# Kernel tuning notes

Measured on AMD Instinct MI355X. Metric: run time of the kernel, lower is better.

The kernel has to match this reference:

```python
import jax, jax.numpy as jnp
import numpy as np

EMBED = 768; HEADS = 12; MLP = 3072
WL_IN = 4        # activation bits (signed)
WL_W = 4         # weight bits (bit-sliced into 1-bit RRAM cells)
ADC = 5          # ADC precision for each analog partial sum
SUBARRAY = 128   # crossbar subArray rows
ONOFF = 10.0     # conductance on/off ratio
VARI = 0.02      # conductance variability
EPS = 1e-5


def _adc_quant(y, bits):
    # Linear ADC quantization over the full observed range.
    ymax = jnp.max(jnp.abs(y))
    step = ymax / (2 ** bits - 1)
    step = jnp.where(step > 0, step, jnp.ones_like(step))
    return jnp.round(y / step) * step


def _qlinear(x, W, b, key):
    # RRAM crossbar simulated linear layer. x: [T, Fin], W: [Fout, Fin].
    upper, lower = 1.0, 1.0 / ONOFF
    T, Fin = x.shape
    Fout = W.shape[0]
    Wlev = 2 ** WL_W - 1
    Xlev = 2 ** (WL_IN - 1) - 1
    # --- weight -> unsigned integer levels -> binary cell conductances ---
    wmax = jnp.max(jnp.abs(W))
    Wdec = jnp.round((W / wmax + 1.0) * 0.5 * Wlev).astype(jnp.int32)   # [Fout,Fin] in [0,Wlev]
    kb = jnp.arange(WL_W)
    wbits = ((Wdec[:, :, None] >> kb) & 1).astype(x.dtype)              # [Fout,Fin,K]
    noise = VARI * jax.random.normal(key, wbits.shape, dtype=x.dtype)   # conductance variability
    cond = (wbits * (upper - lower) + lower) * (1.0 + noise)
    dummy = 0.5 * (upper + lower)                                       # dummy column conductance
    # --- activation -> signed integer -> magnitude bit slices ---
    xmax = jnp.max(jnp.abs(x))
    Xq = jnp.round(x / xmax * Xlev).astype(jnp.int32)
    sgn = jnp.sign(Xq).astype(x.dtype)
    zb = jnp.arange(WL_IN - 1)
    xbits = ((jnp.abs(Xq)[:, :, None] >> zb) & 1).astype(x.dtype) * sgn[:, :, None]  # [T,Fin,Z]
    # --- subArray partitioning along input dim ---
    pad = (-Fin) % SUBARRAY
    if pad:
        xbits = jnp.pad(xbits, ((0, 0), (0, pad), (0, 0)))
        cond = jnp.pad(cond, ((0, 0), (0, pad), (0, 0)))
    nc = (Fin + pad) // SUBARRAY
    xb = xbits.reshape(T, nc, SUBARRAY, WL_IN - 1)
    cb = cond.reshape(Fout, nc, SUBARRAY, WL_W)
    # analog MAC per subarray, per (input bit z, weight cell k)
    partial = jnp.einsum('tcsz,ocsk->tcozk', xb, cb)                    # [T,nc,Fout,Z,K]
    dummyP = dummy * xb.sum(axis=2)                                     # [T,nc,Z]
    partialQ = _adc_quant(partial, ADC)
    dummyQ = _adc_quant(dummyP, ADC)
    net = partialQ - dummyQ[:, :, None, :, None]                        # recenter to signed weights
    scale = (2.0 ** zb)[:, None] * (2.0 ** kb)[None, :]                 # [Z,K] shift-add
    acc = jnp.einsum('tcozk,zk->to', net, scale)
    out = acc * (xmax / Xlev) * (2.0 * wmax / ((upper - lower) * Wlev))
    return out + b


def _layernorm(x, g, b):
    mu = jnp.mean(x, axis=-1, keepdims=True)
    var = jnp.var(x, axis=-1, keepdims=True)
    return (x - mu) * jax.lax.rsqrt(var + EPS) * g + b


def _attention(x, in_w, in_b, out_w, out_b):
    L, N, E = x.shape
    D = E // HEADS
    qkv = x @ in_w.T + in_b                                             # [L,N,3E]
    q, k, v = jnp.split(qkv, 3, axis=-1)
    q = q.reshape(L, N, HEADS, D)
    k = k.reshape(L, N, HEADS, D)
    v = v.reshape(L, N, HEADS, D)
    scores = jnp.einsum('lnhd,mnhd->nhlm', q, k) / jnp.sqrt(jnp.asarray(D, x.dtype))
    attn = jax.nn.softmax(scores, axis=-1)
    ctx = jnp.einsum('nhlm,mnhd->lnhd', attn, v).reshape(L, N, E)
    return ctx @ out_w.T + out_b


def setup_inputs() -> dict:
    key = jax.random.key(0)
    ks = jax.random.split(key, 8)
    s = 0.02
    return {
        'x': jax.random.normal(ks[0], (256, 2, EMBED), jnp.float32),
        'in_proj_w': s * jax.random.normal(ks[1], (3 * EMBED, EMBED), jnp.float32),
        'in_proj_b': jnp.zeros((3 * EMBED,), jnp.float32),
        'out_proj_w': s * jax.random.normal(ks[2], (EMBED, EMBED), jnp.float32),
        'out_proj_b': jnp.zeros((EMBED,), jnp.float32),
        'ln1_g': jnp.ones((EMBED,), jnp.float32),
        'ln1_b': jnp.zeros((EMBED,), jnp.float32),
        'W1': s * jax.random.normal(ks[3], (MLP, EMBED), jnp.float32),
        'b1': jnp.zeros((MLP,), jnp.float32),
        'W2': s * jax.random.normal(ks[4], (EMBED, MLP), jnp.float32),
        'b2': jnp.zeros((EMBED,), jnp.float32),
        'ln2_g': jnp.ones((EMBED,), jnp.float32),
        'ln2_b': jnp.zeros((EMBED,), jnp.float32),
    }


def reference(x, in_proj_w, in_proj_b, out_proj_w, out_proj_b,
              ln1_g, ln1_b, W1, b1, W2, b2, ln2_g, ln2_b):
    L, N, E = x.shape
    a = _attention(x, in_proj_w, in_proj_b, out_proj_w, out_proj_b)
    h = _layernorm(x + a, ln1_g, ln1_b)
    t = h.reshape(L * N, E)
    m = _qlinear(t, W1, b1, jax.random.key(1))
    m = jax.nn.gelu(m, approximate=False)   # torch nn.GELU default = exact erf
    m = _qlinear(m, W2, b2, jax.random.key(2))
    m = m.reshape(L, N, E)
    return _layernorm(h + m, ln2_g, ln2_b)
```

## Files before the change

### kernel.cpp

```cpp
#include <hip/hip_runtime.h>
#include <math.h>
#include <stdint.h>

#define TOK   512
#define EMB   768
#define QKVD  2304
#define NHEAD 12
#define HD    64
#define MLPD  3072
#define SUBA  128

#define OFF_SCAL     0ull
#define OFF_QKV      256ull
#define OFF_SCORES   (OFF_QKV    + 4718592ull)
#define OFF_CTX      (OFF_SCORES + 6291456ull)
#define OFF_H1PRE    (OFF_CTX    + 1572864ull)
#define OFF_H1       (OFF_H1PRE  + 1572864ull)
#define OFF_M1       (OFF_H1     + 1572864ull)
#define OFF_X2       (OFF_M1     + 6291456ull)
#define OFF_M2       (OFF_X2     + 6291456ull)
#define OFF_DQ1      (OFF_M2     + 1572864ull)
#define OFF_DQ2      (OFF_DQ1    + 36864ull)
#define OFF_SUMXB1   (OFF_DQ2    + 147456ull)
#define OFF_SUMXB2   (OFF_SUMXB1 + 36864ull)
#define OFF_WDEC1    (OFF_SUMXB2 + 147456ull)
#define OFF_WDEC2    (OFF_WDEC1  + 2359296ull)
#define OFF_XQT1     (OFF_WDEC2  + 2359296ull)
#define OFF_XQT2     (OFF_XQT1   + 393216ull)
#define OFF_COND1    (OFF_XQT2   + 1572864ull)
#define OFF_COND2    (OFF_COND1  + 37748736ull)
#define WS_NEEDED    (OFF_COND2  + 37748736ull)


typedef float f32x2 __attribute__((ext_vector_type(2)));

__device__ __forceinline__ f32x2 pkfma(f32x2 a, f32x2 b, f32x2 c){
#if __has_builtin(__builtin_elementwise_fma)
  return __builtin_elementwise_fma(a, b, c);
#else
  f32x2 r; r.x = fmaf(a.x, b.x, c.x); r.y = fmaf(a.y, b.y, c.y); return r;
#endif
}

__device__ __forceinline__ void blockMaxAtomic(double v, unsigned long long* slot, double* red){
  int tid = threadIdx.x;
  red[tid] = v; __syncthreads();
  for (int st = 128; st > 0; st >>= 1){
    if (tid < st){ double o = red[tid+st]; if (o > red[tid]) red[tid] = o; }
    __syncthreads();
  }
  if (tid == 0) atomicMax(slot, (unsigned long long)__double_as_longlong(red[0]));
}

__device__ __forceinline__ double readSlot(const unsigned long long* s){
  return __longlong_as_double((long long)(*s));
}

__device__ __forceinline__ float xla_exp_f32(float _x){
  float x = fminf(_x, 88.3762626647950f);
  x = fmaxf(x, -88.3762626647949f);
  float m = floorf(fmaf(x, 1.44269504088896341f, 0.5f));
  float r = fmaf(m, -0.6931471805599453f, x);
  float r2 = __fmul_rn(r, r);
  float r3 = __fmul_rn(r2, r);
  float y  = fmaf(1.9875691500e-4f, r, 1.3981999507e-3f);
  float y1 = fmaf(4.1665795894e-2f, r, 1.6666665459e-1f);
  float y2 = __fadd_rn(r, 1.0f);
  y  = fmaf(y, r, 8.3334519073e-3f);
  y1 = fmaf(y1, r, 5.0000001201e-1f);
  y  = fmaf(y, r3, y1);
  y  = fmaf(y, r2, y2);
  int mi = (int)m;
  float two_m = __uint_as_float((unsigned)((mi + 127) << 23));
  float res = __fmul_rn(y, two_m);
  return fmaxf(res, _x);
}

__device__ __forceinline__ float xla_erf_f32(float v){
  float x = fmaxf(fminf(v, 4.0f), -4.0f);
  float x2 = __fmul_rn(x, x);
  float p = fmaf(x2, -2.72614225801306e-10f, 2.77068142495902e-08f);
  p = fmaf(x2, p, -2.10102402082508e-06f);
  p = fmaf(x2, p, -5.69250639462346e-05f);
  p = fmaf(x2, p, -7.34990630326855e-04f);
  p = fmaf(x2, p, -2.95459980854025e-03f);
  p = fmaf(x2, p, -1.60960333262415e-02f);
  p = __fmul_rn(x, p);
  float q = fmaf(x2, -1.45660718464996e-05f, -2.13374055278905e-04f);
  q = fmaf(x2, q, -1.68282697438203e-03f);
  q = fmaf(x2, q, -7.37332916720468e-03f);
  q = fmaf(x2, q, -1.42647390514189e-02f);
  return __fdiv_rn(p, q);
}

__device__ __forceinline__ uint32_t rotl32(uint32_t x, int r){ return (x << r) | (x >> (32 - r)); }

__device__ __forceinline__ void threefry2x32(uint32_t k0, uint32_t k1,
                                             uint32_t x0, uint32_t x1,
                                             uint32_t& o0, uint32_t& o1){
  uint32_t ks2 = k0 ^ k1 ^ 0x1BD11BDAu;
  x0 += k0; x1 += k1;
#define TF_R(r) { x0 += x1; x1 = rotl32(x1, r); x1 ^= x0; }
  TF_R(13) TF_R(15) TF_R(26) TF_R(6)
  x0 += k1; x1 += ks2 + 1u;
  TF_R(17) TF_R(29) TF_R(16) TF_R(24)
  x0 += ks2; x1 += k0 + 2u;
  TF_R(13) TF_R(15) TF_R(26) TF_R(6)
  x0 += k0; x1 += k1 + 3u;
  TF_R(17) TF_R(29) TF_R(16) TF_R(24)
  x0 += k1; x1 += ks2 + 4u;
  TF_R(13) TF_R(15) TF_R(26) TF_R(6)
  x0 += ks2; x1 += k0 + 5u;
#undef TF_R
  o0 = x0; o1 = x1;
}

__device__ float bits_to_noise(uint32_t bits){
  uint32_t fb = (bits >> 9) | 0x3f800000u;
  float f = __uint_as_float(fb);
  f = __fadd_rn(f, -1.0f);
  const float lo = -0.99999994f;
  float u = __fadd_rn(__fmul_rn(f, 2.0f), lo);
  u = fmaxf(lo, u);
  float x  = u;
  float xx = __fmul_rn(x, x);
  float nx = -xx;
  float l1p;
  if (fabsf(nx) < 1e-4f){
    l1p = __fmul_rn(__fadd_rn(__fmul_rn(-0.5f, nx), 1.0f), nx);
  } else {
    float u1 = __fadd_rn(nx, 1.0f);
    l1p = (float)log((double)u1);
  }
  float w = -l1p;
  float p;
  if (w < 5.0f){
    w = __fadd_rn(w, -2.5f);
    p = 2.81022636e-08f;
    p = __fadd_rn(3.43273939e-07f, __fmul_rn(p, w));
    p = __fadd_rn(-3.5233877e-06f,  __fmul_rn(p, w));
    p = __fadd_rn(-4.39150654e-06f, __fmul_rn(p, w));
    p = __fadd_rn(0.00021858087f,   __fmul_rn(p, w));
    p = __fadd_rn(-0.00125372503f,  __fmul_rn(p, w));
    p = __fadd_rn(-0.00417768164f,  __fmul_rn(p, w));
    p = __fadd_rn(0.246640727f,     __fmul_rn(p, w));
    p = __fadd_rn(1.50140941f,      __fmul_rn(p, w));
  } else {
    float sw = __fsqrt_rn(w);
    w = __fadd_rn(sw, -3.0f);
    p = -0.000200214257f;
    p = __fadd_rn(0.000100950558f, __fmul_rn(p, w));
    p = __fadd_rn(0.00134934322f,  __fmul_rn(p, w));
    p = __fadd_rn(-0.00367342844f, __fmul_rn(p, w));
    p = __fadd_rn(0.00573950773f,  __fmul_rn(p, w));
    p = __fadd_rn(-0.0076224613f,  __fmul_rn(p, w));
    p = __fadd_rn(0.00943887047f,  __fmul_rn(p, w));
    p = __fadd_rn(1.00167406f,     __fmul_rn(p, w));
    p = __fadd_rn(2.83297682f,     __fmul_rn(p, w));
  }
  float ei  = __fmul_rn(p, x);
  float nrm = __fmul_rn(1.41421354f, ei);
  return __fmul_rn(0.02f, nrm);
}

__global__ void absmax_f32_k(const float* p, int n, unsigned long long* slot){
  __shared__ double red[256];
  double m = 0.0;
  for (int i = blockIdx.x*256 + threadIdx.x; i < n; i += gridDim.x*256){
    double v = fabs((double)p[i]); if (v > m) m = v;
  }
  blockMaxAtomic(m, slot, red);
}

__global__ void wdec_gen_k(const float* W, int nW, const unsigned long long* wmax_slot,
                           unsigned char* Wdec){
  int i = blockIdx.x*256 + threadIdx.x;
  if (i >= nW) return;
  float wmax = (float)readSlot(wmax_slot);
  float d = __fdiv_rn(W[i], wmax);
  d = __fadd_rn(d, 1.0f);
  d = __fmul_rn(d, 0.5f);
  d = __fmul_rn(d, 15.0f);
  Wdec[i] = (unsigned char)(int)rintf(d);
}

__global__ void cond_gen_k(uint32_t k0, uint32_t k1, const unsigned char* Wdec,
                           unsigned int n4, float* cond){
  unsigned int j = blockIdx.x*256u + threadIdx.x;
  if (j >= n4) return;
  uint32_t o0, o1;
  threefry2x32(k0, k1, 0u, j, o0, o1);
  float nz = bits_to_noise(o0 ^ o1);
  float bit = (float)((Wdec[j >> 2] >> (j & 3)) & 1);
  cond[j] = __fmul_rn(__fadd_rn(__fmul_rn(bit, 0.9f), 0.1f), __fadd_rn(1.0f, nz));
}

#define KTILE 32
__global__ __launch_bounds__(256) void gemm8_k(const float* src, const float* w, const float* bias,
                                               const float* resid, float* out, int N, int K){
  __shared__ float xt[EMB*8];
  __shared__ float wl[256*(KTILE+1)];
  const int tid = threadIdx.x;
  const int j  = blockIdx.x*256 + tid;
  const int t0 = blockIdx.y*8;
  for (int v = tid; v < K*8; v += 256){
    int e = v >> 3, tt = v & 7;
    xt[v] = src[(size_t)(t0+tt)*K + e];
  }
  f32x2 acc[4] = {{0.f,0.f},{0.f,0.f},{0.f,0.f},{0.f,0.f}};
  const int ntile = K / KTILE;
  for (int et = 0; et < ntile; ++et){
    __syncthreads();
    for (int v = tid; v < 256*KTILE; v += 256){
      int r = v >> 5, cc = v & 31;
      wl[r*(KTILE+1) + cc] = w[(size_t)(blockIdx.x*256 + r)*K + et*KTILE + cc];
    }
    __syncthreads();
    for (int ee = 0; ee < KTILE; ++ee){
      float wv = wl[tid*(KTILE+1) + ee];
      f32x2 wv2 = {wv, wv};
      const f32x2* xp = (const f32x2*)&xt[(et*KTILE + ee)*8];
#pragma unroll
      for (int q = 0; q < 4; ++q) acc[q] = pkfma(xp[q], wv2, acc[q]);
    }
  }
  float bv = bias[j];
#pragma unroll
  for (int q = 0; q < 4; ++q){
    float a0 = __fadd_rn(acc[q].x, bv);
    float a1 = __fadd_rn(acc[q].y, bv);
    size_t ta = (size_t)(t0 + q*2), tb = ta + 1;
    if (resid){
      out[ta*N + j] = __fadd_rn(resid[ta*N + j], a0);
      out[tb*N + j] = __fadd_rn(resid[tb*N + j], a1);
    } else {
      out[ta*N + j] = a0;
      out[tb*N + j] = a1;
    }
  }
}

__global__ __launch_bounds__(256) void attn_scores_k(const float* qkv, float* sc){
  __shared__ float kt[64][34];
  int nh = blockIdx.x;
  int n  = nh / NHEAD, h = nh % NHEAD;
  int m0 = blockIdx.y * 32;
  int l  = threadIdx.x;
  for (int v = threadIdx.x; v < 32*64; v += 256){
    int mm = v >> 6, d = v & 63;
    kt[d][mm] = qkv[(size_t)((m0+mm)*2 + n)*QKVD + EMB + h*HD + d];
  }
  __syncthreads();
  f32x2 acc[16];
#pragma unroll
  for (int i = 0; i < 16; ++i) acc[i] = {0.f,0.f};
  const float* qrow = qkv + (size_t)(l*2 + n)*QKVD + h*HD;
  for (int d = 0; d < HD; ++d){
    float qv = qrow[d];
    f32x2 q2 = {qv, qv};
    const f32x2* kp = (const f32x2*)&kt[d][0];
#pragma unroll
    for (int i = 0; i < 16; ++i) acc[i] = pkfma(q2, kp[i], acc[i]);
  }
  float* srow = sc + ((size_t)nh*256 + l)*256 + m0;
#pragma unroll
  for (int i = 0; i < 16; ++i){
    srow[2*i]   = __fdiv_rn(acc[i].x, 8.0f);
    srow[2*i+1] = __fdiv_rn(acc[i].y, 8.0f);
  }
}

__global__ void softmax_rows_k(float* sc){
  int row = blockIdx.x*256 + threadIdx.x;
  if (row >= 24*256) return;
  float* p = sc + (size_t)row*256;
  float mx = p[0];
  for (int m = 1; m < 256; ++m) mx = fmaxf(mx, p[m]);
  for (int m = 0; m < 256; ++m) p[m] = xla_exp_f32(__fsub_rn(p[m], mx));
  float s = 0.0f;
  for (int m = 0; m < 256; ++m) s = __fadd_rn(s, p[m]);
  for (int m = 0; m < 256; ++m) p[m] = __fdiv_rn(p[m], s);
}

__global__ void attn_ctx_k(const float* sc, const float* qkv, float* ctx){
  int idx = blockIdx.x*256 + threadIdx.x;
  int t = idx / 384, i2 = idx % 384;
  int i = i2*2;
  int l = t >> 1, n = t & 1, h = i >> 6;
  const float* arow = sc + ((size_t)(n*NHEAD + h)*256 + l)*256;
  f32x2 acc = {0.f,0.f};
  for (int m = 0; m < 256; ++m){
    float av = arow[m];
    f32x2 a2 = {av, av};
    f32x2 v2 = *(const f32x2*)&qkv[(size_t)(m*2 + n)*QKVD + 1536 + i];
    acc = pkfma(a2, v2, acc);
  }
  ctx[(size_t)t*EMB + i]     = acc.x;
  ctx[(size_t)t*EMB + i + 1] = acc.y;
}

__global__ void ln_rows_k(const float* in, const float* g, const float* b, float* out){
  int t = blockIdx.x*256 + threadIdx.x;
  if (t >= TOK) return;
  const float* p = in + (size_t)t*EMB;
  float s = 0.0f;
  for (int e = 0; e < EMB; ++e) s = __fadd_rn(s, p[e]);
  float mu = __fdiv_rn(s, 768.0f);
  float s2 = 0.0f;
  for (int e = 0; e < EMB; ++e){
    float d = __fsub_rn(p[e], mu);
    s2 = __fadd_rn(s2, __fmul_rn(d, d));
  }
  float var = __fdiv_rn(s2, 768.0f);
  float rs = __fdiv_rn(1.0f, __fsqrt_rn(__fadd_rn(var, 1e-5f)));
  for (int e = 0; e < EMB; ++e){
    float d = __fsub_rn(p[e], mu);
    out[(size_t)t*EMB + e] = __fadd_rn(__fmul_rn(__fmul_rn(d, rs), g[e]), b[e]);
  }
}

__global__ void final_ln_rows_k(const float* h1, const float* m2T, const float* g, const float* b, float* out){
  int t = blockIdx.x*256 + threadIdx.x;
  if (t >= TOK) return;
  const float* p = h1 + (size_t)t*EMB;
  float s = 0.0f;
  for (int e = 0; e < EMB; ++e) s = __fadd_rn(s, __fadd_rn(p[e], m2T[(size_t)e*TOK + t]));
  float mu = __fdiv_rn(s, 768.0f);
  float s2 = 0.0f;
  for (int e = 0; e < EMB; ++e){
    float d = __fsub_rn(__fadd_rn(p[e], m2T[(size_t)e*TOK + t]), mu);
    s2 = __fadd_rn(s2, __fmul_rn(d, d));
  }
  float var = __fdiv_rn(s2, 768.0f);
  float rs = __fdiv_rn(1.0f, __fsqrt_rn(__fadd_rn(var, 1e-5f)));
  for (int e = 0; e < EMB; ++e){
    float d = __fsub_rn(__fadd_rn(p[e], m2T[(size_t)e*TOK + t]), mu);
    out[(size_t)t*EMB + e] = __fadd_rn(__fmul_rn(__fmul_rn(d, rs), g[e]), b[e]);
  }
}

__device__ __forceinline__ unsigned char encode_q(int q){
  int a = q < 0 ? -q : q;
  int s0 = a & 1, s1 = (a >> 1) & 1, s2 = (a >> 2) & 1;
  if (q < 0){ s0 = -s0; s1 = -s1; s2 = -s2; }
  return (unsigned char)((s0 & 3) | ((s1 & 3) << 2) | ((s2 & 3) << 4));
}

__global__ void quantx_k(const float* val , const unsigned long long* xmax_slot,
                         int Fin, unsigned char* XqT2){
  int idx = blockIdx.x*256 + threadIdx.x;
  if (idx >= TOK*Fin) return;
  int t = idx / Fin, e = idx % Fin;
  float xmax = (float)readSlot(xmax_slot);
  float u = __fmul_rn(__fdiv_rn(val[idx], xmax), 7.0f);
  XqT2[((size_t)(e >> 7)*TOK + t)*SUBA + (e & 127)] = encode_q((int)rintf(u));
}

__global__ void quantxT_k(const float* valT , const unsigned long long* xmax_slot,
                          int Fin, unsigned char* XqT2){
  int idx = blockIdx.x*256 + threadIdx.x;
  if (idx >= TOK*Fin) return;
  int i = idx / TOK, t = idx % TOK;
  float xmax = (float)readSlot(xmax_slot);
  float u = __fmul_rn(__fdiv_rn(valT[idx], xmax), 7.0f);
  XqT2[((size_t)(i >> 7)*TOK + t)*SUBA + (i & 127)] = encode_q((int)rintf(u));
}

__global__ void sumxb_k(const unsigned char* XqT2, int NC, int* sumxb, unsigned long long* dmax_slot){
  int idx = blockIdx.x*256 + threadIdx.x;
  if (idx >= TOK*NC) return;
  int t = idx / NC, c = idx % NC;
  const unsigned char* row = XqT2 + ((size_t)c*TOK + t)*SUBA;
  int n0 = 0, n1 = 0, n2 = 0;
  for (int s = 0; s < SUBA; ++s){
    int e = (int)row[s];
    n0 += ((int)((unsigned)e << 30)) >> 30;
    n1 += ((int)((unsigned)e << 28)) >> 30;
    n2 += ((int)((unsigned)e << 26)) >> 30;
  }
  sumxb[idx*3 + 0] = n0; sumxb[idx*3 + 1] = n1; sumxb[idx*3 + 2] = n2;
  float d0 = fabsf(__fmul_rn(0.55f, (float)n0));
  float d1 = fabsf(__fmul_rn(0.55f, (float)n1));
  float d2 = fabsf(__fmul_rn(0.55f, (float)n2));
  float m = fmaxf(d0, fmaxf(d1, d2));
  atomicMax(dmax_slot, (unsigned long long)__double_as_longlong((double)m));
}

__global__ void dummyq_k(const int* sumxb, int NC, const unsigned long long* dmax_slot, float* dqT){
  int idx = blockIdx.x*256 + threadIdx.x;
  if (idx >= TOK*NC*3) return;
  int t = idx / (NC*3);
  int r = idx % (NC*3);
  int c = r / 3, z = r % 3;
  float dmax = (float)readSlot(dmax_slot);
  float step = __fdiv_rn(dmax, 31.0f);
  if (!(step > 0.0f)) step = 1.0f;
  float P = __fmul_rn(0.55f, (float)sumxb[idx]);
  dqT[((size_t)c*3 + z)*TOK + t] = __fmul_rn(rintf(__fdiv_rn(P, step)), step);
}

template<int OTILE, bool P2, int CCHUNK>
__global__ __launch_bounds__(256) void qlin_k(const unsigned char* XqT2, const float* cond_g,
                                              const float* dqT, const float* bias,
                                              int Fin, int NC,
                                              unsigned long long* ymax_slot,
                                              const unsigned long long* xmax_slot,
                                              const unsigned long long* wmax_slot,
                                              float* outT){
  __shared__ float condL[OTILE*SUBA*4];
  __shared__ double red[P2 ? 1 : 256];
  const int tid = threadIdx.x;
  const int o0 = blockIdx.x*OTILE;
  const int t0 = blockIdx.y*256;
  const int t  = t0 + tid;
  const int c0 = P2 ? 0 : blockIdx.z*CCHUNK;
  const int cEnd = P2 ? NC : (c0 + CCHUNK);

  float step = 1.0f, lmax = 0.0f;
  if (P2){
    float ymax = (float)readSlot(ymax_slot);
    step = __fdiv_rn(ymax, 31.0f);
    if (!(step > 0.0f)) step = 1.0f;
  }

  f32x2 acc[OTILE][6];
  f32x2 netsum[OTILE][6];
  if (P2){
#pragma unroll
    for (int o = 0; o < OTILE; ++o)
#pragma unroll
      for (int r = 0; r < 6; ++r) netsum[o][r] = (f32x2){0.f, 0.f};
  }

#pragma unroll
  for (int u = 0; u < OTILE/2; ++u){
    int v = tid + u*256, o = v >> 7, r = v & 127;
    ((float4*)condL)[v] = ((const float4*)cond_g)[(size_t)(o0+o)*Fin + (size_t)c0*SUBA + r];
  }
  __syncthreads();

  const uint32_t* xrow = (const uint32_t*)(XqT2 + ((size_t)c0*TOK + t)*SUBA);
  uint32_t xg[8];
#pragma unroll
  for (int u = 0; u < 8; ++u) xg[u] = xrow[u];

  for (int c = c0; c < cEnd; ++c){
    const bool haveNextC = (c + 1 < cEnd);
    const uint32_t* xrow_next = haveNextC
      ? (const uint32_t*)(XqT2 + ((size_t)(c+1)*TOK + t)*SUBA) : xrow;

    float4 pf[OTILE/2];
    if (haveNextC){
#pragma unroll
      for (int u = 0; u < OTILE/2; ++u){
        int v = tid + u*256, o = v >> 7, r = v & 127;
        pf[u] = ((const float4*)cond_g)[(size_t)(o0+o)*Fin + (size_t)(c+1)*SUBA + r];
      }
    }

#pragma unroll
    for (int o = 0; o < OTILE; ++o)
#pragma unroll
      for (int r = 0; r < 6; ++r) acc[o][r] = (f32x2){0.f, 0.f};

    for (int g = 0; g < 4; ++g){
      uint32_t xn[8];
      const uint32_t* nsrc = (g < 3) ? (xrow + (g+1)*8) : xrow_next;
#pragma unroll
      for (int u = 0; u < 8; ++u) xn[u] = nsrc[u];
      const float* condG = condL + g*32*4;
#pragma unroll
      for (int u = 0; u < 8; ++u){
        uint32_t w = xg[u];
#pragma unroll
        for (int bb = 0; bb < 4; ++bb){
          int sl = u*4 + bb;
          int base = bb*8;
          int b0i = ((int)(w << (30 - base))) >> 30;
          int b1i = ((int)(w << (28 - base))) >> 30;
          int b2i = ((int)(w << (26 - base))) >> 30;
          float f0 = (float)b0i, f1 = (float)b1i, f2 = (float)b2i;
          f32x2 b0 = {f0, f0}, b1 = {f1, f1}, b2 = {f2, f2};
#pragma unroll
          for (int o = 0; o < OTILE; ++o){
            const f32x2* cp = (const f32x2*)&condG[(o*SUBA + sl)*4];
            f32x2 c01 = cp[0], c23 = cp[1];
            acc[o][0] = pkfma(b0, c01, acc[o][0]);
            acc[o][1] = pkfma(b0, c23, acc[o][1]);
            acc[o][2] = pkfma(b1, c01, acc[o][2]);
            acc[o][3] = pkfma(b1, c23, acc[o][3]);
            acc[o][4] = pkfma(b2, c01, acc[o][4]);
            acc[o][5] = pkfma(b2, c23, acc[o][5]);
          }
        }
      }
#pragma unroll
      for (int u = 0; u < 8; ++u) xg[u] = xn[u];
    }
    xrow = xrow_next;

    if (P2){
      float dqv[3];
#pragma unroll
      for (int z = 0; z < 3; ++z) dqv[z] = dqT[((size_t)c*3 + z)*TOK + t];
#pragma unroll
      for (int o = 0; o < OTILE; ++o)
#pragma unroll
        for (int z = 0; z < 3; ++z)
#pragma unroll
          for (int kp = 0; kp < 2; ++kp){
            f32x2 av = acc[o][z*2 + kp];
            float pq0 = __fmul_rn(rintf(__fdiv_rn(av.x, step)), step);
            float pq1 = __fmul_rn(rintf(__fdiv_rn(av.y, step)), step);
            netsum[o][z*2+kp].x = __fadd_rn(netsum[o][z*2+kp].x, __fsub_rn(pq0, dqv[z]));
            netsum[o][z*2+kp].y = __fadd_rn(netsum[o][z*2+kp].y, __fsub_rn(pq1, dqv[z]));
          }
    } else {
#pragma unroll
      for (int o = 0; o < OTILE; ++o)
#pragma unroll
        for (int r = 0; r < 6; ++r){
          lmax = fmaxf(lmax, fabsf(acc[o][r].x));
          lmax = fmaxf(lmax, fabsf(acc[o][r].y));
        }
    }

    __syncthreads();
    if (haveNextC){
#pragma unroll
      for (int u = 0; u < OTILE/2; ++u)
        ((float4*)condL)[tid + u*256] = pf[u];
      __syncthreads();
    }
  }

  if (P2){
    float xmax = (float)readSlot(xmax_slot);
    float wmax = (float)readSlot(wmax_slot);
    float A = __fdiv_rn(xmax, 7.0f);
    float B = __fdiv_rn(__fmul_rn(2.0f, wmax), 13.5f);
#pragma unroll
    for (int o = 0; o < OTILE; ++o){
      float tot = 0.0f;
#pragma unroll
      for (int z = 0; z < 3; ++z)
#pragma unroll
        for (int k = 0; k < 4; ++k){
          f32x2 ns = netsum[o][z*2 + (k >> 1)];
          float nv = (k & 1) ? ns.y : ns.x;
          tot = __fadd_rn(tot, __fmul_rn(nv, (float)(1 << (z + k))));
        }
      float outv = __fadd_rn(__fmul_rn(__fmul_rn(tot, A), B), bias[o0+o]);
      outT[(size_t)(o0+o)*TOK + t] = outv;
    }
  } else {
    blockMaxAtomic((double)lmax, ymax_slot, red);
  }
}

__global__ void gelu_absmax_k(const float* m1, int n, float* x2, unsigned long long* xmax_slot){
  __shared__ double red[256];
  double m = 0.0;
  for (int i = blockIdx.x*256 + threadIdx.x; i < n; i += gridDim.x*256){
    float v = m1[i];
    float t1 = __fdiv_rn(v, 1.4142135623730951f);
    float e = xla_erf_f32(t1);
    float s = __fadd_rn(e, 1.0f);
    float g = __fdiv_rn(__fmul_rn(v, s), 2.0f);
    x2[i] = g;
    double a = fabs((double)g); if (a > m) m = a;
  }
  blockMaxAtomic(m, xmax_slot, red);
}

extern "C" void kernel_launch(void* const* d_in, const int* in_sizes, int n_in,
                              void* d_out, int out_size, void* d_ws, size_t ws_size,
                              hipStream_t stream){
  if (ws_size < WS_NEEDED) return;
  const float* x      = (const float*)d_in[0];
  const float* in_w   = (const float*)d_in[1];
  const float* in_b   = (const float*)d_in[2];
  const float* out_w  = (const float*)d_in[3];
  const float* out_b  = (const float*)d_in[4];
  const float* ln1_g  = (const float*)d_in[5];
  const float* ln1_b  = (const float*)d_in[6];
  const float* W1     = (const float*)d_in[7];
  const float* b1     = (const float*)d_in[8];
  const float* W2     = (const float*)d_in[9];
  const float* b2     = (const float*)d_in[10];
  const float* ln2_g  = (const float*)d_in[11];
  const float* ln2_b  = (const float*)d_in[12];

  char* ws = (char*)d_ws;
  unsigned long long* scal = (unsigned long long*)(ws + OFF_SCAL);
  float* qkv    = (float*)(ws + OFF_QKV);
  float* scores = (float*)(ws + OFF_SCORES);
  float* ctx    = (float*)(ws + OFF_CTX);
  float* h1pre  = (float*)(ws + OFF_H1PRE);
  float* h1     = (float*)(ws + OFF_H1);
  float* m1     = (float*)(ws + OFF_M1);
  float* x2     = (float*)(ws + OFF_X2);
  float* m2     = (float*)(ws + OFF_M2);
  float* dq1    = (float*)(ws + OFF_DQ1);
  float* dq2    = (float*)(ws + OFF_DQ2);
  int*   sumxb1 = (int*)(ws + OFF_SUMXB1);
  int*   sumxb2 = (int*)(ws + OFF_SUMXB2);
  unsigned char* wdec1 = (unsigned char*)(ws + OFF_WDEC1);
  unsigned char* wdec2 = (unsigned char*)(ws + OFF_WDEC2);
  unsigned char* xqt1 = (unsigned char*)(ws + OFF_XQT1);
  unsigned char* xqt2 = (unsigned char*)(ws + OFF_XQT2);
  float* cond1 = (float*)(ws + OFF_COND1);
  float* cond2 = (float*)(ws + OFF_COND2);

  hipMemsetAsync(scal, 0, 64, stream);

  absmax_f32_k<<<1024,256,0,stream>>>(W1, MLPD*EMB, scal+0);
  absmax_f32_k<<<1024,256,0,stream>>>(W2, EMB*MLPD, scal+1);
  wdec_gen_k<<<9216,256,0,stream>>>(W1, MLPD*EMB, scal+0, wdec1);
  wdec_gen_k<<<9216,256,0,stream>>>(W2, EMB*MLPD, scal+1, wdec2);
  cond_gen_k<<<36864,256,0,stream>>>(0u, 1u, wdec1, 9437184u, cond1);
  cond_gen_k<<<36864,256,0,stream>>>(0u, 2u, wdec2, 9437184u, cond2);

  gemm8_k<<<dim3(9,64),256,0,stream>>>(x, in_w, in_b, nullptr, qkv, QKVD, EMB);
  attn_scores_k<<<dim3(24,8),256,0,stream>>>(qkv, scores);
  softmax_rows_k<<<24,256,0,stream>>>(scores);
  attn_ctx_k<<<768,256,0,stream>>>(scores, qkv, ctx);
  gemm8_k<<<dim3(3,64),256,0,stream>>>(ctx, out_w, out_b, x, h1pre, EMB, EMB);
  ln_rows_k<<<2,256,0,stream>>>(h1pre, ln1_g, ln1_b, h1);

  absmax_f32_k<<<1024,256,0,stream>>>(h1, TOK*EMB, scal+2);
  quantx_k<<<(TOK*EMB+255)/256,256,0,stream>>>(h1, scal+2, EMB, xqt1);
  sumxb_k<<<(TOK*6+255)/256,256,0,stream>>>(xqt1, 6, sumxb1, scal+4);
  dummyq_k<<<(TOK*6*3+255)/256,256,0,stream>>>(sumxb1, 6, scal+4, dq1);
  qlin_k<4,false,3><<<dim3(MLPD/4,2,2),256,0,stream>>>(xqt1, cond1, nullptr, nullptr,
                                                       EMB, 6, scal+3, scal+2, scal+0, nullptr);
  qlin_k<4,true,1><<<dim3(MLPD/4,2),256,0,stream>>>(xqt1, cond1, dq1, b1,
                                                    EMB, 6, scal+3, scal+2, scal+0, m1);

  gelu_absmax_k<<<6144,256,0,stream>>>(m1, TOK*MLPD, x2, scal+5);
  quantxT_k<<<(TOK*MLPD+255)/256,256,0,stream>>>(x2, scal+5, MLPD, xqt2);
  sumxb_k<<<(TOK*24+255)/256,256,0,stream>>>(xqt2, 24, sumxb2, scal+7);
  dummyq_k<<<(TOK*24*3+255)/256,256,0,stream>>>(sumxb2, 24, scal+7, dq2);
  qlin_k<4,false,6><<<dim3(EMB/4,2,4),256,0,stream>>>(xqt2, cond2, nullptr, nullptr,
                                                      MLPD, 24, scal+6, scal+5, scal+1, nullptr);
  qlin_k<2,true,1><<<dim3(EMB/2,2),256,0,stream>>>(xqt2, cond2, dq2, b2,
                                                   MLPD, 24, scal+6, scal+5, scal+1, m2);

  final_ln_rows_k<<<2,256,0,stream>>>(h1, m2, ln2_g, ln2_b, (float*)d_out);
}
```

Baseline: 2.881 ms.

## Cache crossbar partial sums from max pass instead of recomputing them

When the workspace is large enough, the first qlin pass, which finds the ADC range, now writes every per-subarray analog partial sum to a large global buffer. A new combine kernel reads those sums back, ADC-quantizes them, subtracts the dummy column and produces the output, so the second pass no longer redoes the full bit-sliced MAC. This trades the repeated FMA compute for roughly several hundred MB of extra global writes and reads per layer. The shared-memory conductance tile is also accessed as float4. If the workspace is too small, the old two-pass path runs.

```diff
diff --git a/kernel.cpp b/kernel.cpp
--- a/kernel.cpp
+++ b/kernel.cpp
@@ -30,6 +30,8 @@
 #define OFF_COND1    (OFF_XQT2   + 1572864ull)
 #define OFF_COND2    (OFF_COND1  + 37748736ull)
 #define WS_NEEDED    (OFF_COND2  + 37748736ull)
+#define OFF_PART     ((WS_NEEDED + 255ull) & ~255ull)
+#define WS_BIG       (OFF_PART + 452984832ull)
 
 
 typedef float f32x2 __attribute__((ext_vector_type(2)));
@@ -399,15 +401,15 @@
   dqT[((size_t)c*3 + z)*TOK + t] = __fmul_rn(rintf(__fdiv_rn(P, step)), step);
 }
 
-template<int OTILE, bool P2, int CCHUNK>
+template<int OTILE, bool P2, int CCHUNK, bool STORE>
 __global__ __launch_bounds__(256) void qlin_k(const unsigned char* XqT2, const float* cond_g,
                                               const float* dqT, const float* bias,
-                                              int Fin, int NC,
+                                              int Fin, int NC, int Fout,
                                               unsigned long long* ymax_slot,
                                               const unsigned long long* xmax_slot,
                                               const unsigned long long* wmax_slot,
-                                              float* outT){
-  __shared__ float condL[OTILE*SUBA*4];
+                                              float* outT, float* part){
+  __shared__ float4 condL4[OTILE*SUBA];
   __shared__ double red[P2 ? 1 : 256];
   const int tid = threadIdx.x;
   const int o0 = blockIdx.x*OTILE;
@@ -435,7 +437,7 @@
 #pragma unroll
   for (int u = 0; u < OTILE/2; ++u){
     int v = tid + u*256, o = v >> 7, r = v & 127;
-    ((float4*)condL)[v] = ((const float4*)cond_g)[(size_t)(o0+o)*Fin + (size_t)c0*SUBA + r];
+    condL4[v] = ((const float4*)cond_g)[(size_t)(o0+o)*Fin + (size_t)c0*SUBA + r];
   }
   __syncthreads();
 
@@ -468,7 +470,7 @@
       const uint32_t* nsrc = (g < 3) ? (xrow + (g+1)*8) : xrow_next;
 #pragma unroll
       for (int u = 0; u < 8; ++u) xn[u] = nsrc[u];
-      const float* condG = condL + g*32*4;
+      const float4* condG = condL4 + g*32;
 #pragma unroll
       for (int u = 0; u < 8; ++u){
         uint32_t w = xg[u];
@@ -483,8 +485,8 @@
           f32x2 b0 = {f0, f0}, b1 = {f1, f1}, b2 = {f2, f2};
 #pragma unroll
           for (int o = 0; o < OTILE; ++o){
-            const f32x2* cp = (const f32x2*)&condG[(o*SUBA + sl)*4];
-            f32x2 c01 = cp[0], c23 = cp[1];
+            float4 cv = condG[o*SUBA + sl];
+            f32x2 c01 = {cv.x, cv.y}, c23 = {cv.z, cv.w};
             acc[o][0] = pkfma(b0, c01, acc[o][0]);
             acc[o][1] = pkfma(b0, c23, acc[o][1]);
             acc[o][2] = pkfma(b1, c01, acc[o][2]);
@@ -516,6 +518,18 @@
             netsum[o][z*2+kp].y = __fadd_rn(netsum[o][z*2+kp].y, __fsub_rn(pq1, dqv[z]));
           }
     } else {
+      if (STORE){
+        size_t base = ((size_t)c*Fout + o0)*12;
+#pragma unroll
+        for (int o = 0; o < OTILE; ++o)
+#pragma unroll
+          for (int z = 0; z < 3; ++z)
+#pragma unroll
+            for (int kp = 0; kp < 2; ++kp){
+              part[(base + o*12 + z*4 + kp*2    )*TOK + t] = acc[o][z*2+kp].x;
+              part[(base + o*12 + z*4 + kp*2 + 1)*TOK + t] = acc[o][z*2+kp].y;
+            }
+      }
 #pragma unroll
       for (int o = 0; o < OTILE; ++o)
 #pragma unroll
@@ -529,7 +543,7 @@
     if (haveNextC){
 #pragma unroll
       for (int u = 0; u < OTILE/2; ++u)
-        ((float4*)condL)[tid + u*256] = pf[u];
+        condL4[tid + u*256] = pf[u];
       __syncthreads();
     }
   }
@@ -555,6 +569,63 @@
     }
   } else {
     blockMaxAtomic((double)lmax, ymax_slot, red);
+  }
+}
+
+template<int OTILE>
+__global__ __launch_bounds__(256) void qlin2c_k(const float* part, const float* dqT, const float* bias,
+                                                int Fout, int NC,
+                                                const unsigned long long* ymax_slot,
+                                                const unsigned long long* xmax_slot,
+                                                const unsigned long long* wmax_slot,
+                                                float* outT){
+  const int tid = threadIdx.x;
+  const int o0 = blockIdx.x*OTILE;
+  const int t  = blockIdx.y*256 + tid;
+  float ymax = (float)readSlot(ymax_slot);
+  float step = __fdiv_rn(ymax, 31.0f);
+  if (!(step > 0.0f)) step = 1.0f;
+  f32x2 netsum[OTILE][6];
+#pragma unroll
+  for (int o = 0; o < OTILE; ++o)
+#pragma unroll
+    for (int r = 0; r < 6; ++r) netsum[o][r] = (f32x2){0.f, 0.f};
+  for (int c = 0; c < NC; ++c){
+    float dqv[3];
+#pragma unroll
+    for (int z = 0; z < 3; ++z) dqv[z] = dqT[((size_t)c*3 + z)*TOK + t];
+    size_t base = ((size_t)c*Fout + o0)*12;
+#pragma unroll
+    for (int o = 0; o < OTILE; ++o)
+#pragma unroll
+      for (int z = 0; z < 3; ++z)
+#pragma unroll
+        for (int kp = 0; kp < 2; ++kp){
+          float p0 = part[(base + o*12 + z*4 + kp*2    )*TOK + t];
+          float p1 = part[(base + o*12 + z*4 + kp*2 + 1)*TOK + t];
+          float pq0 = __fmul_rn(rintf(__fdiv_rn(p0, step)), step);
+          float pq1 = __fmul_rn(rintf(__fdiv_rn(p1, step)), step);
+          netsum[o][z*2+kp].x = __fadd_rn(netsum[o][z*2+kp].x, __fsub_rn(pq0, dqv[z]));
+          netsum[o][z*2+kp].y = __fadd_rn(netsum[o][z*2+kp].y, __fsub_rn(pq1, dqv[z]));
+        }
+  }
+  float xmax = (float)readSlot(xmax_slot);
+  float wmax = (float)readSlot(wmax_slot);
+  float A = __fdiv_rn(xmax, 7.0f);
+  float B = __fdiv_rn(__fmul_rn(2.0f, wmax), 13.5f);
+#pragma unroll
+  for (int o = 0; o < OTILE; ++o){
+    float tot = 0.0f;
+#pragma unroll
+    for (int z = 0; z < 3; ++z)
+#pragma unroll
+      for (int k = 0; k < 4; ++k){
+        f32x2 ns = netsum[o][z*2 + (k >> 1)];
+        float nv = (k & 1) ? ns.y : ns.x;
+        tot = __fadd_rn(tot, __fmul_rn(nv, (float)(1 << (z + k))));
+      }
+    float outv = __fadd_rn(__fmul_rn(__fmul_rn(tot, A), B), bias[o0+o]);
+    outT[(size_t)(o0+o)*TOK + t] = outv;
   }
 }
 
@@ -577,6 +648,8 @@
                               void* d_out, int out_size, void* d_ws, size_t ws_size,
                               hipStream_t stream){
   if (ws_size < WS_NEEDED) return;
+  const bool big = (ws_size >= WS_BIG);
+
   const float* x      = (const float*)d_in[0];
   const float* in_w   = (const float*)d_in[1];
   const float* in_b   = (const float*)d_in[2];
@@ -611,6 +684,7 @@
   unsigned char* xqt2 = (unsigned char*)(ws + OFF_XQT2);
   float* cond1 = (float*)(ws + OFF_COND1);
   float* cond2 = (float*)(ws + OFF_COND2);
+  float* part  = (float*)(ws + OFF_PART);
 
   hipMemsetAsync(scal, 0, 64, stream);
 
@@ -632,19 +706,33 @@
   quantx_k<<<(TOK*EMB+255)/256,256,0,stream>>>(h1, scal+2, EMB, xqt1);
   sumxb_k<<<(TOK*6+255)/256,256,0,stream>>>(xqt1, 6, sumxb1, scal+4);
   dummyq_k<<<(TOK*6*3+255)/256,256,0,stream>>>(sumxb1, 6, scal+4, dq1);
-  qlin_k<4,false,3><<<dim3(MLPD/4,2,2),256,0,stream>>>(xqt1, cond1, nullptr, nullptr,
-                                                       EMB, 6, scal+3, scal+2, scal+0, nullptr);
-  qlin_k<4,true,1><<<dim3(MLPD/4,2),256,0,stream>>>(xqt1, cond1, dq1, b1,
-                                                    EMB, 6, scal+3, scal+2, scal+0, m1);
+  if (big){
+    qlin_k<4,false,3,true><<<dim3(MLPD/4,2,2),256,0,stream>>>(xqt1, cond1, nullptr, nullptr,
+        EMB, 6, MLPD, scal+3, scal+2, scal+0, nullptr, part);
+    qlin2c_k<1><<<dim3(MLPD,2),256,0,stream>>>(part, dq1, b1, MLPD, 6,
+        scal+3, scal+2, scal+0, m1);
+  } else {
+    qlin_k<4,false,3,false><<<dim3(MLPD/4,2,2),256,0,stream>>>(xqt1, cond1, nullptr, nullptr,
+        EMB, 6, MLPD, scal+3, scal+2, scal+0, nullptr, nullptr);
+    qlin_k<4,true,1,false><<<dim3(MLPD/4,2),256,0,stream>>>(xqt1, cond1, dq1, b1,
+        EMB, 6, MLPD, scal+3, scal+2, scal+0, m1, nullptr);
+  }
 
   gelu_absmax_k<<<6144,256,0,stream>>>(m1, TOK*MLPD, x2, scal+5);
   quantxT_k<<<(TOK*MLPD+255)/256,256,0,stream>>>(x2, scal+5, MLPD, xqt2);
   sumxb_k<<<(TOK*24+255)/256,256,0,stream>>>(xqt2, 24, sumxb2, scal+7);
   dummyq_k<<<(TOK*24*3+255)/256,256,0,stream>>>(sumxb2, 24, scal+7, dq2);
-  qlin_k<4,false,6><<<dim3(EMB/4,2,4),256,0,stream>>>(xqt2, cond2, nullptr, nullptr,
-                                                      MLPD, 24, scal+6, scal+5, scal+1, nullptr);
-  qlin_k<2,true,1><<<dim3(EMB/2,2),256,0,stream>>>(xqt2, cond2, dq2, b2,
-                                                   MLPD, 24, scal+6, scal+5, scal+1, m2);
+  if (big){
+    qlin_k<4,false,6,true><<<dim3(EMB/4,2,4),256,0,stream>>>(xqt2, cond2, nullptr, nullptr,
+        MLPD, 24, EMB, scal+6, scal+5, scal+1, nullptr, part);
+    qlin2c_k<1><<<dim3(EMB,2),256,0,stream>>>(part, dq2, b2, EMB, 24,
+        scal+6, scal+5, scal+1, m2);
+  } else {
+    qlin_k<4,false,6,false><<<dim3(EMB/4,2,4),256,0,stream>>>(xqt2, cond2, nullptr, nullptr,
+        MLPD, 24, EMB, scal+6, scal+5, scal+1, nullptr, nullptr);
+    qlin_k<2,true,1,false><<<dim3(EMB/2,2),256,0,stream>>>(xqt2, cond2, dq2, b2,
+        MLPD, 24, EMB, scal+6, scal+5, scal+1, m2, nullptr);
+  }
 
   final_ln_rows_k<<<2,256,0,stream>>>(h1, m2, ln2_g, ln2_b, (float*)d_out);
 }
```

New measurement: 2.997 ms. +4.1%, slower.
